# Optimization experiments

Measured on AMD Instinct MI355X. Metric: run time of the kernel, lower is better.

The kernel has to match this reference:

```python
import jax, jax.numpy as jnp
import numpy as np

B = 1024          # batch
D = 6             # data_dim
H = 128           # hidden_dim
VW = 256          # vf_hidden_dim (MLP width and output)
LS = 22           # logsig_dim (first entry dropped in vector field)
NI = 64           # number of log-signature intervals
NSTEPS = 64       # fixed Heun steps over [0, 1]


def setup_inputs() -> dict:
    key = jax.random.key(0)
    ks = jax.random.split(key, 12)
    ts = jnp.linspace(0.0, 1.0, NI + 1, dtype=jnp.float32)
    logsig = 0.1 * jax.random.normal(ks[0], (B, NI, LS), dtype=jnp.float32)
    x0 = jax.random.normal(ks[1], (B, D), dtype=jnp.float32)
    def lin(k, out_d, in_d):
        s = 1.0 / np.sqrt(in_d)
        kw, kb = jax.random.split(k)
        W = jax.random.uniform(kw, (out_d, in_d), jnp.float32, -s, s)
        b = jax.random.uniform(kb, (out_d,), jnp.float32, -s, s)
        return W, b
    W_vf1, b_vf1 = lin(ks[2], VW, H)    # VectorField MLP: hidden -> width
    W_vf2, b_vf2 = lin(ks[3], VW, VW)   # width -> vf out, final tanh
    Wm, bm = lin(ks[4], H * (LS - 1), VW)  # mlp_linear
    W1, b1 = lin(ks[5], H, D)           # linear1
    W2, b2 = lin(ks[6], 10, H)          # linear2 (label_dim=10)
    return {"ts": ts, "logsig": logsig, "x0": x0,
            "W_vf1": W_vf1, "b_vf1": b_vf1, "W_vf2": W_vf2, "b_vf2": b_vf2,
            "Wm": Wm, "bm": bm, "W1": W1, "b1": b1, "W2": W2, "b2": b2}


def reference(ts, logsig, x0, W_vf1, b_vf1, W_vf2, b_vf2, Wm, bm, W1, b1, W2, b2):
    intervals = ts                      # breakpoints, shape (NI+1,)
    dt = (ts[-1] - ts[0]) / NSTEPS
    ls_tail = logsig[:, :, 1:]          # (B, NI, LS-1), drop leading logsig term

    def vf(y):                          # VectorField MLP, batched: (B,H)->(B,VW)
        h = jax.nn.relu(jnp.einsum("bh,wh->bw", y, W_vf1) + b_vf1)
        return jnp.tanh(jnp.einsum("bw,vw->bv", h, W_vf2) + b_vf2)

    def func(t, y):                     # dy/dt, shape (B, H)
        idx = jnp.clip(jnp.searchsorted(intervals, t), 1, NI)
        A = (jnp.einsum("bv,ov->bo", vf(y), Wm) + bm).reshape(-1, H, LS - 1)
        ls = ls_tail[:, idx - 1]        # (B, LS-1)
        width = intervals[idx] - intervals[idx - 1]
        return jnp.einsum("bhl,bl->bh", A, ls) / width

    def heun_step(y, t):
        k1 = func(t, y)
        k2 = func(t + dt, y + dt * k1)
        return y + 0.5 * dt * (k1 + k2), None

    y0 = jnp.einsum("bd,hd->bh", x0, W1) + b1
    step_ts = ts[0] + dt * jnp.arange(NSTEPS, dtype=jnp.float32)
    yT, _ = jax.lax.scan(heun_step, y0, step_ts)
    return jax.nn.softmax(jnp.einsum("bh,ch->bc", yT, W2) + b2, axis=-1)
```

## Files before the change

### kernel.cpp

```cpp
#include <hip/hip_runtime.h>
#include <hip/hip_bf16.h>

typedef float f32x4 __attribute__((ext_vector_type(4)));
typedef int   i32x4 __attribute__((ext_vector_type(4)));
typedef short s16x8 __attribute__((ext_vector_type(8)));
typedef unsigned short u16;

#define NGP 32
#define BT 16
#define NWG 256
#define NTH 512
#define PREPTH 256
#define H 128
#define VW 256
#define NI 64
#define NSTEPS 64

#define OFF_FRAG16 0
#define OFF_WMQ    196608
#define OFF_BMF    884736
#define OFF_SCF    895488
#define OFF_SINV   896000
#define OFF_YBUF   896512
#define YBUF_BYTES 1048576

#define MFMA_BF16(a,b,c) __builtin_amdgcn_mfma_f32_16x16x32_bf16(a,b,c,0,0,0)
#define MFMA_I8(a,b,c)   __builtin_amdgcn_mfma_i32_16x16x64_i8(a,b,c,0,0,0)

__device__ __forceinline__ u16 bf16u(float f) {
  union { float f; unsigned u; } x; x.f = f;
  return (u16)((x.u + 0x7fffu + ((x.u >> 16) & 1u)) >> 16);
}
__device__ __forceinline__ float b2f(u16 u) {
  union { unsigned u; float f; } x; x.u = ((unsigned)u) << 16;
  return x.f;
}

__global__ void prep_scales(const float* __restrict__ Wm, char* __restrict__ ws) {
  __shared__ float red[4];
  const int tid = threadIdx.x;
  const int h = blockIdx.x;
  float m = 0.f;
  for (int i = tid; i < 21 * VW; i += PREPTH) m = fmaxf(m, fabsf(Wm[h * 21 * VW + i]));
  for (int off = 32; off > 0; off >>= 1) m = fmaxf(m, __shfl_down(m, off));
  if ((tid & 63) == 0) red[tid >> 6] = m;
  __syncthreads();
  if (tid == 0) {
    m = fmaxf(fmaxf(red[0], red[1]), fmaxf(red[2], red[3]));
    m = fmaxf(m, 1e-20f);
    ((float*)(ws + OFF_SCF))[h]  = m / 16129.f;
    ((float*)(ws + OFF_SINV))[h] = 127.f / m;
  }
}

__global__ void prep_pack(const float* __restrict__ Wvf1, const float* __restrict__ Wvf2,
                          const float* __restrict__ Wm, const float* __restrict__ bmv,
                          char* __restrict__ ws) {
  int idx = blockIdx.x * blockDim.x + threadIdx.x;
  if (idx < 98304) {
    u16* w16 = (u16*)(ws + OFF_FRAG16);
    float val;
    if (idx < 32768) {
      int e = idx;
      int j = e & 7, ln = (e >> 3) & 63, nt = (e >> 9) & 15, kk = e >> 13;
      val = Wvf1[(nt * 16 + (ln & 15)) * H + kk * 32 + (ln >> 4) * 8 + j];
    } else {
      int e = idx - 32768;
      int j = e & 7, ln = (e >> 3) & 63, nt = (e >> 9) & 15, kk = e >> 13;
      val = Wvf2[(nt * 16 + (ln & 15)) * VW + kk * 32 + (ln >> 4) * 8 + j];
    }
    w16[idx] = bf16u(val);
  } else if (idx < 98304 + 688128) {
    int b = idx - 98304;
    int j = b & 15, lane = (b >> 4) & 63, kk = (b >> 10) & 3, rem = b >> 12;
    int l = rem % 21, nt = rem / 21;
    int h = nt * 16 + (lane & 15);
    int w = kk * 64 + (lane >> 4) * 16 + j;
    float sinv = ((const float*)(ws + OFF_SINV))[h];
    float val = Wm[(size_t)(h * 21 + l) * VW + w];
    int q = (int)lrintf(val * sinv);
    q = min(127, max(-127, q));
    ((signed char*)(ws + OFF_WMQ))[b] = (signed char)q;
  } else if (idx < 98304 + 688128 + 2688) {
    int b = idx - (98304 + 688128);
    int hh = b & 15, rem = b >> 4;
    int l = rem % 21, nt = rem / 21;
    ((float*)(ws + OFF_BMF))[b] = bmv[(nt * 16 + hh) * 21 + l];
  }
}

__global__ __launch_bounds__(NTH, 1) void rde_main(
    const float* __restrict__ logsig, const float* __restrict__ x0,
    const float* __restrict__ W1, const float* __restrict__ b1,
    const float* __restrict__ bvf1, const float* __restrict__ bvf2,
    const float* __restrict__ W2, const float* __restrict__ b2,
    char* __restrict__ ws, float* __restrict__ out) {
  __shared__ __align__(16) signed char WmL[86016];
  __shared__ __align__(16) u16   YB [2][BT][H + 8];
  __shared__ __align__(16) u16   V1F[4096];
  __shared__ __align__(16) signed char V2QH[4096];
  __shared__ __align__(16) float LSF[2][2][21][BT];
  __shared__ __align__(16) float part[8][BT][17];
  __shared__ __align__(16) float bmL[336];
  __shared__ float scL[16];
  __shared__ float LG[32][10];

  const int tid = threadIdx.x;
  const int lane = tid & 63;
  const int wv = tid >> 6;
  const int c = lane & 15;
  const int kg = lane >> 4;
  const int bid = blockIdx.x;
  const int Gp = (bid & 7) * 4 + (bid >> 6);
  const int t = (bid >> 3) & 7;
  const int b0 = Gp * 32;
  unsigned* __restrict__ ybuf = (unsigned*)(ws + OFF_YBUF);
  const s16x8* __restrict__ fr16 = (const s16x8*)(ws + OFF_FRAG16);
  const f32x4 zf = {0.f, 0.f, 0.f, 0.f};
  const i32x4 zi = {0, 0, 0, 0};

  s16x8 w1r[2][4], w2r[2][8];
#pragma unroll
  for (int n = 0; n < 2; ++n) {
#pragma unroll
    for (int kk = 0; kk < 4; ++kk) w1r[n][kk] = fr16[(kk * 16 + wv * 2 + n) * 64 + lane];
#pragma unroll
    for (int kk = 0; kk < 8; ++kk) w2r[n][kk] = fr16[4096 + (kk * 16 + wv * 2 + n) * 64 + lane];
  }
  f32x4 bv1v[2], bv2v[2];
#pragma unroll
  for (int n = 0; n < 2; ++n) {
    bv1v[n] = *(const f32x4*)&bvf1[wv * 32 + n * 16 + kg * 4];
    bv2v[n] = *(const f32x4*)&bvf2[wv * 32 + n * 16 + kg * 4];
  }

  {
    const i32x4* wsrc = (const i32x4*)(ws + OFF_WMQ + t * 86016);
    i32x4* wdst = (i32x4*)WmL;
    for (int e = tid; e < 5376; e += NTH) wdst[e] = wsrc[e];
  }
  if (tid < 16) scL[tid] = ((const float*)(ws + OFF_SCF))[t * 16 + tid];
  if (tid < 336) bmL[tid] = ((const float*)(ws + OFF_BMF))[t * 336 + tid];

  for (int e = tid; e < 2 * BT * H; e += NTH) {
    int tt = e >> 11, r = (e >> 7) & 15, h = e & 127;
    float a = b1[h];
#pragma unroll
    for (int d = 0; d < 6; ++d) a += x0[(b0 + tt * 16 + r) * 6 + d] * W1[h * 6 + d];
    YB[tt][r][h] = bf16u(a);
  }
  float y0s = 0.f, y1s = 0.f, yp0s = 0.f, yp1s = 0.f;
  float bmd0 = 0.f, bmd1 = 0.f;
  if (tid < 256) {
    int r = tid >> 4, hh = tid & 15, h = t * 16 + hh;
    float a0 = b1[h], a1 = b1[h];
#pragma unroll
    for (int d = 0; d < 6; ++d) {
      a0 += x0[(b0 + r) * 6 + d] * W1[h * 6 + d];
      a1 += x0[(b0 + 16 + r) * 6 + d] * W1[h * 6 + d];
    }
    y0s = a0; y1s = a1;
  }

  auto STAGE = [&](int T, int iv) {
    if (tid < BT * 21) {
      int r = tid / 21, l = tid - r * 21;
      LSF[T][iv & 1][l][r] = logsig[((size_t)(b0 + T * 16 + r) * NI + iv) * 22 + 1 + l];
    }
  };
  auto S1 = [&](int T) {
    s16x8 ay0 = *(const s16x8*)&YB[T][c][0 * 32 + kg * 8];
    s16x8 ay1 = *(const s16x8*)&YB[T][c][1 * 32 + kg * 8];
    s16x8 ay2 = *(const s16x8*)&YB[T][c][2 * 32 + kg * 8];
    s16x8 ay3 = *(const s16x8*)&YB[T][c][3 * 32 + kg * 8];
    f32x4 pA = MFMA_BF16(w1r[0][0], ay0, zf), pB = MFMA_BF16(w1r[1][0], ay0, zf);
    pA = MFMA_BF16(w1r[0][1], ay1, pA);  pB = MFMA_BF16(w1r[1][1], ay1, pB);
    pA = MFMA_BF16(w1r[0][2], ay2, pA);  pB = MFMA_BF16(w1r[1][2], ay2, pB);
    pA = MFMA_BF16(w1r[0][3], ay3, pA);  pB = MFMA_BF16(w1r[1][3], ay3, pB);
#pragma unroll
    for (int n = 0; n < 2; ++n) {
      f32x4 p = n ? pB : pA;
      unsigned lo = (unsigned)bf16u(fmaxf(p[0] + bv1v[n][0], 0.f)) |
                    ((unsigned)bf16u(fmaxf(p[1] + bv1v[n][1], 0.f)) << 16);
      unsigned hi = (unsigned)bf16u(fmaxf(p[2] + bv1v[n][2], 0.f)) |
                    ((unsigned)bf16u(fmaxf(p[3] + bv1v[n][3], 0.f)) << 16);
      int u64i = ((wv * 4 + n * 2 + (kg >> 1)) * 16 + c) * 2 + (kg & 1);
      ((unsigned long long*)V1F)[u64i] =
          (unsigned long long)lo | ((unsigned long long)hi << 32);
    }
  };
  auto S2 = [&]() {
    const s16x8* v1f8 = (const s16x8*)V1F;
    s16x8 av0 = v1f8[(0 * 4 + kg) * 16 + c];
    s16x8 av1 = v1f8[(1 * 4 + kg) * 16 + c];
    s16x8 av2 = v1f8[(2 * 4 + kg) * 16 + c];
    s16x8 av3 = v1f8[(3 * 4 + kg) * 16 + c];
    s16x8 av4 = v1f8[(4 * 4 + kg) * 16 + c];
    s16x8 av5 = v1f8[(5 * 4 + kg) * 16 + c];
    s16x8 av6 = v1f8[(6 * 4 + kg) * 16 + c];
    s16x8 av7 = v1f8[(7 * 4 + kg) * 16 + c];
    f32x4 pA = MFMA_BF16(w2r[0][0], av0, zf), pB = MFMA_BF16(w2r[1][0], av0, zf);
    pA = MFMA_BF16(w2r[0][1], av1, pA);  pB = MFMA_BF16(w2r[1][1], av1, pB);
    pA = MFMA_BF16(w2r[0][2], av2, pA);  pB = MFMA_BF16(w2r[1][2], av2, pB);
    pA = MFMA_BF16(w2r[0][3], av3, pA);  pB = MFMA_BF16(w2r[1][3], av3, pB);
    pA = MFMA_BF16(w2r[0][4], av4, pA);  pB = MFMA_BF16(w2r[1][4], av4, pB);
    pA = MFMA_BF16(w2r[0][5], av5, pA);  pB = MFMA_BF16(w2r[1][5], av5, pB);
    pA = MFMA_BF16(w2r[0][6], av6, pA);  pB = MFMA_BF16(w2r[1][6], av6, pB);
    pA = MFMA_BF16(w2r[0][7], av7, pA);  pB = MFMA_BF16(w2r[1][7], av7, pB);
#pragma unroll
    for (int n = 0; n < 2; ++n) {
      f32x4 p = n ? pB : pA;
      unsigned wq = 0;
#pragma unroll
      for (int q = 0; q < 4; ++q) {
        float x = p[q] + bv2v[n][q];
        float e2 = __expf(2.f * x);
        float t127 = fmaf(-254.f, __builtin_amdgcn_rcpf(e2 + 1.f), 127.f);
        wq |= ((unsigned)((int)rintf(t127) & 255)) << (q * 8);
      }
      ((unsigned*)V2QH)[((2 * wv + n) * 16 + c) * 4 + kg] = wq;
    }
  };
  auto S3 = [&](int T, int lsb_) {
    i32x4 aih0 = *(const i32x4*)&V2QH[(0 * 64 + lane) * 16];
    i32x4 aih1 = *(const i32x4*)&V2QH[(1 * 64 + lane) * 16];
    i32x4 aih2 = *(const i32x4*)&V2QH[(2 * 64 + lane) * 16];
    i32x4 aih3 = *(const i32x4*)&V2QH[(3 * 64 + lane) * 16];
    const int nl = (wv < 5) ? 3 : 2;
    const int lb = (wv < 5) ? 3 * wv : 15 + 2 * (wv - 5);
    f32x4 acc = zf;
    for (int li = 0; li < nl; ++li) {
      int l = lb + li;
      const i32x4* bp = (const i32x4*)WmL + l * 256 + lane;
      i32x4 bq0 = bp[0], bq1 = bp[64], bq2 = bp[128], bq3 = bp[192];
      i32x4 PH = MFMA_I8(aih0, bq0, zi);
      PH = MFMA_I8(aih1, bq1, PH);
      PH = MFMA_I8(aih2, bq2, PH);
      PH = MFMA_I8(aih3, bq3, PH);
      f32x4 ls4 = *(const f32x4*)&LSF[T][lsb_][l][kg * 4];
#pragma unroll
      for (int q = 0; q < 4; ++q) acc[q] += ls4[q] * (float)PH[q];
    }
#pragma unroll
    for (int q = 0; q < 4; ++q) part[wv][kg * 4 + q][c] = acc[q];
  };
  auto S4 = [&](int T, int jj, int lsb_, float& y, float& yp, float& bmdc) {
    if (tid < 256) {
      int r = tid >> 4, hh = tid & 15;
      float s = ((part[0][r][hh] + part[1][r][hh]) + (part[2][r][hh] + part[3][r][hh])) +
                ((part[4][r][hh] + part[5][r][hh]) + (part[6][r][hh] + part[7][r][hh]));
      if (jj == 0 || (jj & 1)) {
        float bmd = 0.f;
#pragma unroll
        for (int l = 0; l < 21; ++l) bmd += LSF[T][lsb_][l][r] * bmL[l * 16 + hh];
        bmdc = bmd;
      }
      float raw = scL[hh] * s + bmdc;
      float yn;
      if (!(jj & 1)) { yp = y + 0.5f * raw; yn = y + raw; }
      else           { y = yp + 0.5f * raw; yn = y; }
      unsigned v = ((unsigned)(jj + 1) << 16) | (unsigned)bf16u(yn);
      __hip_atomic_store(&ybuf[((Gp * 2 + T) * 2 + (jj & 1)) * 2048 + r * 128 + t * 16 + hh],
                         v, __ATOMIC_RELAXED, __HIP_MEMORY_SCOPE_AGENT);
    }
  };
  auto S5 = [&](int T, int jj) {
    const unsigned tg = (unsigned)(jj + 1);
    const unsigned* pb = ybuf + ((Gp * 2 + T) * 2 + (jj & 1)) * 2048;
    unsigned v0, v1, v2, v3;
#pragma unroll 1
    for (int sp = 0; sp < 60000; ++sp) {
      v0 = __hip_atomic_load(&pb[tid],        __ATOMIC_RELAXED, __HIP_MEMORY_SCOPE_AGENT);
      v1 = __hip_atomic_load(&pb[tid + 512],  __ATOMIC_RELAXED, __HIP_MEMORY_SCOPE_AGENT);
      v2 = __hip_atomic_load(&pb[tid + 1024], __ATOMIC_RELAXED, __HIP_MEMORY_SCOPE_AGENT);
      v3 = __hip_atomic_load(&pb[tid + 1536], __ATOMIC_RELAXED, __HIP_MEMORY_SCOPE_AGENT);
      unsigned mn = min(min(v0 >> 16, v1 >> 16), min(v2 >> 16, v3 >> 16));
      if (mn == tg) break;
    }
    YB[T][tid >> 7][tid & 127] = (u16)(v0 & 0xffffu);
    YB[T][(tid + 512) >> 7][(tid + 512) & 127] = (u16)(v1 & 0xffffu);
    YB[T][(tid + 1024) >> 7][(tid + 1024) & 127] = (u16)(v2 & 0xffffu);
    YB[T][(tid + 1536) >> 7][(tid + 1536) & 127] = (u16)(v3 & 0xffffu);
  };

  __syncthreads();

  STAGE(1, 0);
  __syncthreads();
  S1(1);
  __syncthreads();
  S2();
  __syncthreads();

#pragma unroll 1
  for (int j = 0; j < 2 * NSTEPS; ++j) {
    const int step_ = j >> 1, sub_ = j & 1;
    const int lsb_ = (sub_ ? step_ : (step_ > 0 ? step_ - 1 : 0)) & 1;
    if (!sub_) STAGE(0, step_);
    S1(0);
    S3(1, lsb_);
    __syncthreads();
    S4(1, j, lsb_, y1s, yp1s, bmd1);
    S2();
    S5(1, j);
    __syncthreads();
    S3(0, lsb_);
    if (j < 2 * NSTEPS - 1) {
      if (sub_) STAGE(1, (j + 1) >> 1);
      S1(1);
    }
    __syncthreads();
    S4(0, j, lsb_, y0s, yp0s, bmd0);
    if (j < 2 * NSTEPS - 1) S2();
    S5(0, j);
    __syncthreads();
  }

  if (t == 0) {
    for (int e = tid; e < 32 * 10; e += NTH) {
      int rr = e / 10, cc = e - rr * 10;
      float a = b2[cc];
#pragma unroll 4
      for (int h = 0; h < H; ++h) a += b2f(YB[rr >> 4][rr & 15][h]) * W2[cc * H + h];
      LG[rr][cc] = a;
    }
    __syncthreads();
    if (tid < 32) {
      float mx = -1e30f;
#pragma unroll
      for (int cc = 0; cc < 10; ++cc) mx = fmaxf(mx, LG[tid][cc]);
      float ex[10]; float s = 0.f;
#pragma unroll
      for (int cc = 0; cc < 10; ++cc) { ex[cc] = expf(LG[tid][cc] - mx); s += ex[cc]; }
      float inv = 1.f / s;
#pragma unroll
      for (int cc = 0; cc < 10; ++cc) out[(b0 + tid) * 10 + cc] = ex[cc] * inv;
    }
  }
}

extern "C" void kernel_launch(void* const* d_in, const int* in_sizes, int n_in,
                              void* d_out, int out_size, void* d_ws, size_t ws_size,
                              hipStream_t stream) {
  (void)in_sizes; (void)n_in; (void)out_size; (void)ws_size;
  const float* logsig = (const float*)d_in[1];
  const float* x0     = (const float*)d_in[2];
  const float* Wvf1   = (const float*)d_in[3];
  const float* bvf1   = (const float*)d_in[4];
  const float* Wvf2   = (const float*)d_in[5];
  const float* bvf2   = (const float*)d_in[6];
  const float* Wm     = (const float*)d_in[7];
  const float* bmv    = (const float*)d_in[8];
  const float* W1     = (const float*)d_in[9];
  const float* b1     = (const float*)d_in[10];
  const float* W2     = (const float*)d_in[11];
  const float* b2     = (const float*)d_in[12];
  char* ws = (char*)d_ws;

  prep_scales<<<128, PREPTH, 0, stream>>>(Wm, ws);
  prep_pack<<<3083, PREPTH, 0, stream>>>(Wvf1, Wvf2, Wm, bmv, ws);
  hipMemsetAsync(ws + OFF_YBUF, 0, YBUF_BYTES, stream);
  rde_main<<<NWG, NTH, 0, stream>>>(logsig, x0, W1, b1, bvf1, bvf2, W2, b2, ws,
                                    (float*)d_out);
}
```

Baseline: 600.0 us.

## Pipeline four batch tiles across stages with double-buffered shared staging

Each workgroup now handles 64 batch rows split into four 16-row tiles instead of two, and the launch grid drops to 128 workgroups. The per-step work is restructured into a 4-phase software pipeline, where each phase runs S1/S2/S3/S45 on different tiles. The intermediate shared buffers are double-buffered so each phase needs only one barrier. The aim is to hide cross-workgroup spin-wait latency and barrier stalls behind independent tile work, at the cost of fewer, more heavily loaded workgroups, more shared memory and more registers.

```diff
diff --git a/kernel.cpp b/kernel.cpp
--- a/kernel.cpp
+++ b/kernel.cpp
@@ -6,9 +6,9 @@
 typedef short s16x8 __attribute__((ext_vector_type(8)));
 typedef unsigned short u16;
 
-#define NGP 32
+#define NGP 16
 #define BT 16
-#define NWG 256
+#define NWG 128
 #define NTH 512
 #define PREPTH 256
 #define H 128
@@ -96,14 +96,13 @@
     const float* __restrict__ W2, const float* __restrict__ b2,
     char* __restrict__ ws, float* __restrict__ out) {
   __shared__ __align__(16) signed char WmL[86016];
-  __shared__ __align__(16) u16   YB [2][BT][H + 8];
-  __shared__ __align__(16) u16   V1F[4096];
-  __shared__ __align__(16) signed char V2QH[4096];
-  __shared__ __align__(16) float LSF[2][2][21][BT];
-  __shared__ __align__(16) float part[8][BT][17];
+  __shared__ __align__(16) u16   YB [4][BT][H + 8];
+  __shared__ __align__(16) u16   V1F[2][4096];
+  __shared__ __align__(16) signed char V2Q[2][4096];
+  __shared__ __align__(16) float LSF[4][2][21][BT];
+  __shared__ __align__(16) float part[2][8][BT][17];
   __shared__ __align__(16) float bmL[336];
   __shared__ float scL[16];
-  __shared__ float LG[32][10];
 
   const int tid = threadIdx.x;
   const int lane = tid & 63;
@@ -111,9 +110,9 @@
   const int c = lane & 15;
   const int kg = lane >> 4;
   const int bid = blockIdx.x;
-  const int Gp = (bid & 7) * 4 + (bid >> 6);
-  const int t = (bid >> 3) & 7;
-  const int b0 = Gp * 32;
+  const int Gp = bid & 15;
+  const int t = bid >> 4;
+  const int b0 = Gp * 64;
   unsigned* __restrict__ ybuf = (unsigned*)(ws + OFF_YBUF);
   const s16x8* __restrict__ fr16 = (const s16x8*)(ws + OFF_FRAG16);
   const f32x4 zf = {0.f, 0.f, 0.f, 0.f};
@@ -142,33 +141,34 @@
   if (tid < 16) scL[tid] = ((const float*)(ws + OFF_SCF))[t * 16 + tid];
   if (tid < 336) bmL[tid] = ((const float*)(ws + OFF_BMF))[t * 336 + tid];
 
-  for (int e = tid; e < 2 * BT * H; e += NTH) {
+  for (int e = tid; e < 4 * BT * H; e += NTH) {
     int tt = e >> 11, r = (e >> 7) & 15, h = e & 127;
     float a = b1[h];
 #pragma unroll
     for (int d = 0; d < 6; ++d) a += x0[(b0 + tt * 16 + r) * 6 + d] * W1[h * 6 + d];
     YB[tt][r][h] = bf16u(a);
   }
-  float y0s = 0.f, y1s = 0.f, yp0s = 0.f, yp1s = 0.f;
-  float bmd0 = 0.f, bmd1 = 0.f;
+  float y_st[4], yp_st[4], bmdc[4];
+#pragma unroll
+  for (int i = 0; i < 4; ++i) { y_st[i] = 0.f; yp_st[i] = 0.f; bmdc[i] = 0.f; }
   if (tid < 256) {
     int r = tid >> 4, hh = tid & 15, h = t * 16 + hh;
-    float a0 = b1[h], a1 = b1[h];
-#pragma unroll
-    for (int d = 0; d < 6; ++d) {
-      a0 += x0[(b0 + r) * 6 + d] * W1[h * 6 + d];
-      a1 += x0[(b0 + 16 + r) * 6 + d] * W1[h * 6 + d];
-    }
-    y0s = a0; y1s = a1;
-  }
-
-  auto STAGE = [&](int T, int iv) {
-    if (tid < BT * 21) {
+#pragma unroll
+    for (int tt = 0; tt < 4; ++tt) {
+      float a = b1[h];
+#pragma unroll
+      for (int d = 0; d < 6; ++d) a += x0[(b0 + tt * 16 + r) * 6 + d] * W1[h * 6 + d];
+      y_st[tt] = a;
+    }
+  }
+  __syncthreads();
+
+  auto S1 = [&](int T, int jj, int W) {
+    if ((jj & 1) == 0 && tid < BT * 21) {
       int r = tid / 21, l = tid - r * 21;
-      LSF[T][iv & 1][l][r] = logsig[((size_t)(b0 + T * 16 + r) * NI + iv) * 22 + 1 + l];
-    }
-  };
-  auto S1 = [&](int T) {
+      LSF[T][(jj >> 1) & 1][l][r] =
+          logsig[((size_t)(b0 + T * 16 + r) * NI + (jj >> 1)) * 22 + 1 + l];
+    }
     s16x8 ay0 = *(const s16x8*)&YB[T][c][0 * 32 + kg * 8];
     s16x8 ay1 = *(const s16x8*)&YB[T][c][1 * 32 + kg * 8];
     s16x8 ay2 = *(const s16x8*)&YB[T][c][2 * 32 + kg * 8];
@@ -185,12 +185,12 @@
       unsigned hi = (unsigned)bf16u(fmaxf(p[2] + bv1v[n][2], 0.f)) |
                     ((unsigned)bf16u(fmaxf(p[3] + bv1v[n][3], 0.f)) << 16);
       int u64i = ((wv * 4 + n * 2 + (kg >> 1)) * 16 + c) * 2 + (kg & 1);
-      ((unsigned long long*)V1F)[u64i] =
+      ((unsigned long long*)&V1F[W][0])[u64i] =
           (unsigned long long)lo | ((unsigned long long)hi << 32);
     }
   };
-  auto S2 = [&]() {
-    const s16x8* v1f8 = (const s16x8*)V1F;
+  auto S2 = [&](int R, int W) {
+    const s16x8* v1f8 = (const s16x8*)&V1F[R][0];
     s16x8 av0 = v1f8[(0 * 4 + kg) * 16 + c];
     s16x8 av1 = v1f8[(1 * 4 + kg) * 16 + c];
     s16x8 av2 = v1f8[(2 * 4 + kg) * 16 + c];
@@ -218,14 +218,16 @@
         float t127 = fmaf(-254.f, __builtin_amdgcn_rcpf(e2 + 1.f), 127.f);
         wq |= ((unsigned)((int)rintf(t127) & 255)) << (q * 8);
       }
-      ((unsigned*)V2QH)[((2 * wv + n) * 16 + c) * 4 + kg] = wq;
+      ((unsigned*)&V2Q[W][0])[((2 * wv + n) * 16 + c) * 4 + kg] = wq;
     }
   };
-  auto S3 = [&](int T, int lsb_) {
-    i32x4 aih0 = *(const i32x4*)&V2QH[(0 * 64 + lane) * 16];
-    i32x4 aih1 = *(const i32x4*)&V2QH[(1 * 64 + lane) * 16];
-    i32x4 aih2 = *(const i32x4*)&V2QH[(2 * 64 + lane) * 16];
-    i32x4 aih3 = *(const i32x4*)&V2QH[(3 * 64 + lane) * 16];
+  auto S3 = [&](int T, int jj, int R, int W) {
+    int step = jj >> 1;
+    int lsb = ((jj & 1) ? step : (step > 0 ? step - 1 : 0)) & 1;
+    i32x4 aih0 = *(const i32x4*)&V2Q[R][(0 * 64 + lane) * 16];
+    i32x4 aih1 = *(const i32x4*)&V2Q[R][(1 * 64 + lane) * 16];
+    i32x4 aih2 = *(const i32x4*)&V2Q[R][(2 * 64 + lane) * 16];
+    i32x4 aih3 = *(const i32x4*)&V2Q[R][(3 * 64 + lane) * 16];
     const int nl = (wv < 5) ? 3 : 2;
     const int lb = (wv < 5) ? 3 * wv : 15 + 2 * (wv - 5);
     f32x4 acc = zf;
@@ -237,36 +239,38 @@
       PH = MFMA_I8(aih1, bq1, PH);
       PH = MFMA_I8(aih2, bq2, PH);
       PH = MFMA_I8(aih3, bq3, PH);
-      f32x4 ls4 = *(const f32x4*)&LSF[T][lsb_][l][kg * 4];
+      f32x4 ls4 = *(const f32x4*)&LSF[T][lsb][l][kg * 4];
 #pragma unroll
       for (int q = 0; q < 4; ++q) acc[q] += ls4[q] * (float)PH[q];
     }
 #pragma unroll
-    for (int q = 0; q < 4; ++q) part[wv][kg * 4 + q][c] = acc[q];
+    for (int q = 0; q < 4; ++q) part[W][wv][kg * 4 + q][c] = acc[q];
   };
-  auto S4 = [&](int T, int jj, int lsb_, float& y, float& yp, float& bmdc) {
+  auto S45 = [&](int T, int jj, int R, float& y, float& yp, float& bmd) {
+    int step = jj >> 1;
+    int lsb = ((jj & 1) ? step : (step > 0 ? step - 1 : 0)) & 1;
     if (tid < 256) {
       int r = tid >> 4, hh = tid & 15;
-      float s = ((part[0][r][hh] + part[1][r][hh]) + (part[2][r][hh] + part[3][r][hh])) +
-                ((part[4][r][hh] + part[5][r][hh]) + (part[6][r][hh] + part[7][r][hh]));
+      float s = ((part[R][0][r][hh] + part[R][1][r][hh]) +
+                 (part[R][2][r][hh] + part[R][3][r][hh])) +
+                ((part[R][4][r][hh] + part[R][5][r][hh]) +
+                 (part[R][6][r][hh] + part[R][7][r][hh]));
       if (jj == 0 || (jj & 1)) {
-        float bmd = 0.f;
-#pragma unroll
-        for (int l = 0; l < 21; ++l) bmd += LSF[T][lsb_][l][r] * bmL[l * 16 + hh];
-        bmdc = bmd;
+        float bm = 0.f;
+#pragma unroll
+        for (int l = 0; l < 21; ++l) bm += LSF[T][lsb][l][r] * bmL[l * 16 + hh];
+        bmd = bm;
       }
-      float raw = scL[hh] * s + bmdc;
+      float raw = scL[hh] * s + bmd;
       float yn;
       if (!(jj & 1)) { yp = y + 0.5f * raw; yn = y + raw; }
       else           { y = yp + 0.5f * raw; yn = y; }
       unsigned v = ((unsigned)(jj + 1) << 16) | (unsigned)bf16u(yn);
-      __hip_atomic_store(&ybuf[((Gp * 2 + T) * 2 + (jj & 1)) * 2048 + r * 128 + t * 16 + hh],
+      __hip_atomic_store(&ybuf[((Gp * 4 + T) * 2 + (jj & 1)) * 2048 + r * 128 + t * 16 + hh],
                          v, __ATOMIC_RELAXED, __HIP_MEMORY_SCOPE_AGENT);
     }
-  };
-  auto S5 = [&](int T, int jj) {
     const unsigned tg = (unsigned)(jj + 1);
-    const unsigned* pb = ybuf + ((Gp * 2 + T) * 2 + (jj & 1)) * 2048;
+    const unsigned* pb = ybuf + ((Gp * 4 + T) * 2 + (jj & 1)) * 2048;
     unsigned v0, v1, v2, v3;
 #pragma unroll 1
     for (int sp = 0; sp < 60000; ++sp) {
@@ -283,55 +287,52 @@
     YB[T][(tid + 1536) >> 7][(tid + 1536) & 127] = (u16)(v3 & 0xffffu);
   };
 
-  __syncthreads();
-
-  STAGE(1, 0);
-  __syncthreads();
-  S1(1);
-  __syncthreads();
-  S2();
-  __syncthreads();
+#define PHASE(rr, TA, TC, TD)                                                  \
+  {                                                                            \
+    const int Wp = (rr) & 1, Rp = Wp ^ 1;                                      \
+    if (q < 2 * NSTEPS) S1(TA, q, Wp);                                         \
+    {                                                                          \
+      int j2 = ((rr) >= 1) ? q : q - 1;                                        \
+      if (j2 >= 0 && j2 < 2 * NSTEPS) S2(Rp, Wp);                              \
+    }                                                                          \
+    {                                                                          \
+      int j3 = ((rr) >= 2) ? q : q - 1;                                        \
+      if (j3 >= 0 && j3 < 2 * NSTEPS) S3(TC, j3, Rp, Wp);                      \
+    }                                                                          \
+    {                                                                          \
+      int j4 = ((rr) >= 3) ? q : q - 1;                                        \
+      if (j4 >= 0 && j4 < 2 * NSTEPS)                                          \
+        S45(TD, j4, Rp, y_st[TD], yp_st[TD], bmdc[TD]);                        \
+    }                                                                          \
+    __syncthreads();                                                           \
+  }
 
 #pragma unroll 1
-  for (int j = 0; j < 2 * NSTEPS; ++j) {
-    const int step_ = j >> 1, sub_ = j & 1;
-    const int lsb_ = (sub_ ? step_ : (step_ > 0 ? step_ - 1 : 0)) & 1;
-    if (!sub_) STAGE(0, step_);
-    S1(0);
-    S3(1, lsb_);
-    __syncthreads();
-    S4(1, j, lsb_, y1s, yp1s, bmd1);
-    S2();
-    S5(1, j);
-    __syncthreads();
-    S3(0, lsb_);
-    if (j < 2 * NSTEPS - 1) {
-      if (sub_) STAGE(1, (j + 1) >> 1);
-      S1(1);
-    }
-    __syncthreads();
-    S4(0, j, lsb_, y0s, yp0s, bmd0);
-    if (j < 2 * NSTEPS - 1) S2();
-    S5(0, j);
-    __syncthreads();
-  }
-
+  for (int q = 0; q <= 2 * NSTEPS; ++q) {
+    PHASE(0, 0, 2, 1)
+    PHASE(1, 1, 3, 2)
+    PHASE(2, 2, 0, 3)
+    PHASE(3, 3, 1, 0)
+  }
+#undef PHASE
+
+  float* LG = (float*)part;
   if (t == 0) {
-    for (int e = tid; e < 32 * 10; e += NTH) {
+    for (int e = tid; e < 64 * 10; e += NTH) {
       int rr = e / 10, cc = e - rr * 10;
       float a = b2[cc];
 #pragma unroll 4
       for (int h = 0; h < H; ++h) a += b2f(YB[rr >> 4][rr & 15][h]) * W2[cc * H + h];
-      LG[rr][cc] = a;
+      LG[rr * 10 + cc] = a;
     }
     __syncthreads();
-    if (tid < 32) {
+    if (tid < 64) {
       float mx = -1e30f;
 #pragma unroll
-      for (int cc = 0; cc < 10; ++cc) mx = fmaxf(mx, LG[tid][cc]);
+      for (int cc = 0; cc < 10; ++cc) mx = fmaxf(mx, LG[tid * 10 + cc]);
       float ex[10]; float s = 0.f;
 #pragma unroll
-      for (int cc = 0; cc < 10; ++cc) { ex[cc] = expf(LG[tid][cc] - mx); s += ex[cc]; }
+      for (int cc = 0; cc < 10; ++cc) { ex[cc] = expf(LG[tid * 10 + cc] - mx); s += ex[cc]; }
       float inv = 1.f / s;
 #pragma unroll
       for (int cc = 0; cc < 10; ++cc) out[(b0 + tid) * 10 + cc] = ex[cc] * inv;
```

After: 1.587 ms. 2.64x slower.
